# Performance work log

Measured on AMD Instinct MI355X. Metric: run time of the kernel, lower is better.

Reference implementation:

```python
import jax, jax.numpy as jnp
import numpy as np
from jax import lax

BLOCK = 20  # hardcoded block_size in BlockSparseSelfAttention
HEADS = 8
LAYERS = 4
EPS = 1e-5


def _ln(x, g, b):
    m = jnp.mean(x, axis=-1, keepdims=True)
    v = jnp.mean(jnp.square(x - m), axis=-1, keepdims=True)
    return (x - m) * lax.rsqrt(v + EPS) * g + b


def _conv1d(x_nct, w, b):
    # x: (B,C,T), w: (O,I,3) -> (B,O,T), padding=1 == SAME for k=3
    y = lax.conv_general_dilated(x_nct, w, (1,), 'SAME',
                                 dimension_numbers=('NCH', 'OIH', 'NCH'))
    return y + b[None, :, None]


def _block_attn(x, in_w, in_b, out_w, out_b):
    # torch nn.MultiheadAttention applied independently per length-BLOCK chunk
    B, T, D = x.shape
    nb, hd = T // BLOCK, D // HEADS
    xb = x.reshape(B, nb, BLOCK, D)
    qkv = jnp.einsum('bnsd,ed->bnse', xb, in_w) + in_b  # e = 3D
    q, k, v = jnp.split(qkv, 3, axis=-1)
    q = q.reshape(B, nb, BLOCK, HEADS, hd)
    k = k.reshape(B, nb, BLOCK, HEADS, hd)
    v = v.reshape(B, nb, BLOCK, HEADS, hd)
    scale = jnp.asarray(1.0 / np.sqrt(hd), x.dtype)
    s = jnp.einsum('bnqhd,bnkhd->bnhqk', q, k) * scale
    a = jax.nn.softmax(s, axis=-1)
    o = jnp.einsum('bnhqk,bnkhd->bnqhd', a, v).reshape(B, nb, BLOCK, D)
    o = jnp.einsum('bnsd,od->bnso', o, out_w) + out_b
    return o.reshape(B, T, D)


def setup_inputs() -> dict:
    key = jax.random.key(0)
    ks = iter(jax.random.split(key, 16))
    B, T, C, D, L = 32, 4000, 16, 256, LAYERS
    F = 4 * D
    s_c = 1.0 / np.sqrt(C * 3)
    s_d = 1.0 / np.sqrt(D)
    s_d3 = 1.0 / np.sqrt(D * 3)
    s_f = 1.0 / np.sqrt(F)
    f32 = jnp.float32
    return {
        'x': jax.random.normal(next(ks), (B, T, C), f32),
        'conv1_w': jax.random.normal(next(ks), (D, C, 3), f32) * s_c,
        'conv1_b': jnp.zeros((D,), f32),
        'conv2_w': jax.random.normal(next(ks), (D, D, 3), f32) * s_d3,
        'conv2_b': jnp.zeros((D,), f32),
        'ln_f_g': jnp.ones((D,), f32), 'ln_f_b': jnp.zeros((D,), f32),
        'trend_w': jax.random.normal(next(ks), (D, D), f32) * s_d,
        'trend_b': jnp.zeros((D,), f32),
        'season_w': jax.random.normal(next(ks), (D, D), f32) * s_d,
        'season_b': jnp.zeros((D,), f32),
        'attn_in_w': jax.random.normal(next(ks), (L, 3 * D, D), f32) * s_d,
        'attn_in_b': jnp.zeros((L, 3 * D), f32),
        'attn_out_w': jax.random.normal(next(ks), (L, D, D), f32) * s_d,
        'attn_out_b': jnp.zeros((L, D), f32),
        'ln1_g': jnp.ones((L, D), f32), 'ln1_b': jnp.zeros((L, D), f32),
        'ff1_w': jax.random.normal(next(ks), (L, F, D), f32) * s_d,
        'ff1_b': jnp.zeros((L, F), f32),
        'ff2_w': jax.random.normal(next(ks), (L, D, F), f32) * s_f,
        'ff2_b': jnp.zeros((L, D), f32),
        'ln2_g': jnp.ones((L, D), f32), 'ln2_b': jnp.zeros((L, D), f32),
        'fc_w': jax.random.normal(next(ks), (C, D), f32) * s_d,
        'fc_b': jnp.zeros((C,), f32),
    }


def reference(x, conv1_w, conv1_b, conv2_w, conv2_b, ln_f_g, ln_f_b,
              trend_w, trend_b, season_w, season_b,
              attn_in_w, attn_in_b, attn_out_w, attn_out_b,
              ln1_g, ln1_b, ff1_w, ff1_b, ff2_w, ff2_b, ln2_g, ln2_b,
              fc_w, fc_b):
    # FeatureExtractor
    h = x.transpose(0, 2, 1)                       # (B,C,T)
    h = jax.nn.relu(_conv1d(h, conv1_w, conv1_b))
    h = jax.nn.relu(_conv1d(h, conv2_w, conv2_b))
    h = h.transpose(0, 2, 1)                       # (B,T,D)
    h = _ln(h, ln_f_g, ln_f_b)
    # trend + seasonality residual
    h = h + (h @ trend_w.T + trend_b) + jnp.sin(h @ season_w.T + season_b)
    # encoder stack (dropout disabled / eval mode)
    for i in range(LAYERS):
        a = _block_attn(h, attn_in_w[i], attn_in_b[i], attn_out_w[i], attn_out_b[i])
        h = _ln(h + a, ln1_g[i], ln1_b[i])
        f = jax.nn.relu(h @ ff1_w[i].T + ff1_b[i]) @ ff2_w[i].T + ff2_b[i]
        h = _ln(h + f, ln2_g[i], ln2_b[i])
    return h[:, -1, :] @ fc_w.T + fc_b             # (B,C)
```

## Files before the change

### kernel.cpp

```cpp
#include <hip/hip_runtime.h>
#include <math.h>

typedef __attribute__((ext_vector_type(8))) short short8;
typedef __attribute__((ext_vector_type(4))) short short4v;
typedef __attribute__((ext_vector_type(4))) float f32x4;
typedef unsigned short ushort;
typedef unsigned int uint;
typedef unsigned long long u64;

#define MFMA16(a, b, c) __builtin_amdgcn_mfma_f32_16x16x32_bf16(a, b, c, 0, 0, 0)

__device__ __forceinline__ ushort f2bf(float f) {
  uint u = __float_as_uint(f);
  u = (u + 0x7FFFu + ((u >> 16) & 1u)) >> 16;
  return (ushort)u;
}
__device__ __forceinline__ int swz(int idx, int sh) {
  return idx ^ (((idx >> sh) & 7) << 3);
}
__device__ __forceinline__ float wsum(float v) {
#pragma unroll
  for (int off = 32; off > 0; off >>= 1) v += __shfl_xor(v, off, 64);
  return v;
}
__device__ __forceinline__ void gload16(short8& dst, const ushort* g) {
  u64 ga = (u64)g;
  asm volatile("global_load_dwordx4 %0, %1, off" : "=v"(dst) : "v"(ga));
}
__device__ __forceinline__ void vmw(int n) {
  if (n >= 7) asm volatile("s_waitcnt vmcnt(7)" ::: "memory");
  else if (n == 6) asm volatile("s_waitcnt vmcnt(6)" ::: "memory");
  else if (n == 5) asm volatile("s_waitcnt vmcnt(5)" ::: "memory");
  else if (n == 4) asm volatile("s_waitcnt vmcnt(4)" ::: "memory");
  else if (n == 3) asm volatile("s_waitcnt vmcnt(3)" ::: "memory");
  else if (n == 2) asm volatile("s_waitcnt vmcnt(2)" ::: "memory");
  else if (n == 1) asm volatile("s_waitcnt vmcnt(1)" ::: "memory");
  else asm volatile("s_waitcnt vmcnt(0)" ::: "memory");
}

#define S_CONV2 0
#define S_TREND 196608
#define S_SEASON 262144
#define S_QKV 327680
#define S_AOW 1114112
#define S_F1 1376256
#define S_F2 2424832
#define WTOT 3473408
#define O_C1G 3473408
#define O_C2O 3653632
#define O_G0 3981312
#define O_G1 4308992
#define O_PEND 4636672
#define O_QKV 4964352
#define O_FFB 5455872

template <int NCH>
__device__ __forceinline__ void dec2(int idx, int& row, int& k) {
  int pos = idx & 511, lane = pos >> 3, j = pos & 7;
  int kg = lane >> 4, col = lane & 15;
  int chunk = idx >> 9;
  int tile = chunk / (NCH * 4), r = chunk - tile * (NCH * 4);
  int kc = r >> 2, ks = r & 3;
  row = tile * 16 + col;
  k = kc * 128 + ks * 32 + kg * 8 + j;
}

__global__ void k_cvt(const float* __restrict__ c2w, const float* __restrict__ tw,
                      const float* __restrict__ sw, const float* __restrict__ aiw,
                      const float* __restrict__ aow, const float* __restrict__ f1w,
                      const float* __restrict__ f2w, ushort* __restrict__ ws) {
  for (int i = blockIdx.x * blockDim.x + threadIdx.x; i < WTOT;
       i += gridDim.x * blockDim.x) {
    float v; int row, k;
    if (i < S_TREND) {
      dec2<6>(i, row, k);
      int t = k >> 8, e = k & 255;
      v = c2w[row * 768 + e * 3 + t];
    } else if (i < S_SEASON) { dec2<2>(i - S_TREND, row, k); v = tw[row * 256 + k]; }
    else if (i < S_QKV) { dec2<2>(i - S_SEASON, row, k); v = sw[row * 256 + k]; }
    else if (i < S_AOW) {
      int r = i - S_QKV; int l = r / 196608; r -= l * 196608;
      dec2<2>(r, row, k); v = aiw[(size_t)l * 196608 + row * 256 + k];
    } else if (i < S_F1) {
      int r = i - S_AOW; int l = r >> 16; r &= 65535;
      dec2<2>(r, row, k); v = aow[l * 65536 + row * 256 + k];
    } else if (i < S_F2) {
      int r = i - S_F1; int l = r >> 18; r &= 262143;
      dec2<2>(r, row, k); v = f1w[l * 262144 + row * 256 + k];
    } else {
      int r = i - S_F2; int l = r >> 18; r &= 262143;
      dec2<8>(r, row, k); v = f2w[l * 262144 + row * 1024 + k];
    }
    ws[i] = f2bf(v);
  }
}

template <int NCH, int MY, int ASH>
__device__ __forceinline__ void ring_gemm(const ushort* __restrict__ A, int lda,
                                          const ushort* __restrict__ ws0,
                                          int lane, f32x4 (&acc)[MY][2]) {
  constexpr int C = MY * NCH * 4;
  constexpr int R = (C < 8) ? C : 8;
  const int col = lane & 15, kg = lane >> 4;
  const int r1c = (16 + col > 19) ? 19 : (16 + col);
  short8 rg[R];
#pragma unroll
  for (int r = 0; r < R; ++r) gload16(rg[r], ws0 + r * 512);
  short8 af0[4], af1[4];
#pragma unroll
  for (int c = 0; c < C; ++c) {
    const int i = c / (NCH * 4), r = c - i * (NCH * 4);
    const int kc = r >> 2, ks = r & 3;
    if (ks == 0) {
#pragma unroll
      for (int s = 0; s < 4; ++s) {
        const int k0 = kc * 128 + s * 32 + kg * 8;
        af0[s] = *(const short8*)(A + swz(col * lda + k0, ASH));
        af1[s] = *(const short8*)(A + swz(r1c * lda + k0, ASH));
      }
    }
    int allow = C - 1 - c; if (allow > R - 1) allow = R - 1;
    vmw(allow);
    __builtin_amdgcn_sched_barrier(0);
    acc[i][0] = MFMA16(af0[ks], rg[c % R], acc[i][0]);
    acc[i][1] = MFMA16(af1[ks], rg[c % R], acc[i][1]);
    if (c + R < C) gload16(rg[c % R], ws0 + (c + R) * 512);
  }
}

__device__ __forceinline__ void stage_b16(const ushort* __restrict__ g, ushort* hb,
                                          int n, int sh, int tid) {
  for (int i = tid * 8; i < n; i += 2048) {
    short8 v = *(const short8*)(g + i);
    *(short8*)(hb + swz(i, sh)) = v;
  }
}
__device__ __forceinline__ void stage_f32(const float* __restrict__ g, ushort* hb, int tid) {
  for (int i = tid * 8; i < 5120; i += 2048) {
    float4 a = *(const float4*)(g + i);
    float4 b = *(const float4*)(g + i + 4);
    short8 t;
    t[0] = f2bf(a.x); t[1] = f2bf(a.y); t[2] = f2bf(a.z); t[3] = f2bf(a.w);
    t[4] = f2bf(b.x); t[5] = f2bf(b.y); t[6] = f2bf(b.z); t[7] = f2bf(b.w);
    *(short8*)(hb + swz(i, 8)) = t;
  }
}
__device__ __forceinline__ void stage_ln(const float* __restrict__ g1,
                                         const float* __restrict__ pend,
                                         const float* __restrict__ gam,
                                         const float* __restrict__ bet,
                                         ushort* hb, float* __restrict__ gout,
                                         float* f32lds, int tid) {
  const int lane = tid & 63, w = tid >> 6, d0 = lane * 4;
  for (int r = w; r < 20; r += 4) {
    float4 a = *(const float4*)(g1 + r * 256 + d0);
    if (pend) {
      float4 p = *(const float4*)(pend + r * 256 + d0);
      a.x += p.x; a.y += p.y; a.z += p.z; a.w += p.w;
    }
    float m = wsum(a.x + a.y + a.z + a.w) * (1.f / 256.f);
    float c0 = a.x - m, c1 = a.y - m, c2 = a.z - m, c3 = a.w - m;
    float var = wsum(c0 * c0 + c1 * c1 + c2 * c2 + c3 * c3) * (1.f / 256.f);
    float inv = rsqrtf(var + 1e-5f);
    float o0 = c0 * inv * gam[d0] + bet[d0];
    float o1 = c1 * inv * gam[d0 + 1] + bet[d0 + 1];
    float o2 = c2 * inv * gam[d0 + 2] + bet[d0 + 2];
    float o3 = c3 * inv * gam[d0 + 3] + bet[d0 + 3];
    short4v t; t[0] = f2bf(o0); t[1] = f2bf(o1); t[2] = f2bf(o2); t[3] = f2bf(o3);
    *(short4v*)(hb + swz(r * 256 + d0, 8)) = t;
    if (gout) { float4 o = {o0, o1, o2, o3}; *(float4*)(gout + r * 256 + d0) = o; }
    if (f32lds) { float4 o = {o0, o1, o2, o3}; *(float4*)(f32lds + r * 256 + d0) = o; }
  }
}

__global__ __launch_bounds__(256) void k_conv1(const float* __restrict__ x,
                                               const float* __restrict__ c1w,
                                               const float* __restrict__ c1b,
                                               ushort* __restrict__ c1g) {
  __shared__ float xs[24][16];
  const int tid = threadIdx.x, b = blockIdx.x;
  for (int i = tid; i < 24 * 16; i += 256) {
    int r = i >> 4, c = i & 15;
    xs[r][c] = (r < 23) ? x[((size_t)b * 4000 + 3977 + r) * 16 + c] : 0.f;
  }
  __syncthreads();
  const int d = tid;
  const float* wr = c1w + d * 48;
  float acc[21];
  const float bv = c1b[d];
#pragma unroll
  for (int r = 0; r < 21; ++r) acc[r] = bv;
  for (int c = 0; c < 16; ++c) {
    float xv[23];
#pragma unroll
    for (int i = 0; i < 23; ++i) xv[i] = xs[i + 1][c];
    float w0 = wr[c * 3], w1 = wr[c * 3 + 1], w2 = wr[c * 3 + 2];
#pragma unroll
    for (int r = 0; r < 21; ++r)
      acc[r] += xv[r] * w0 + xv[r + 1] * w1 + xv[r + 2] * w2;
  }
  ushort* o = c1g + b * 5632;
#pragma unroll
  for (int r = 0; r < 21; ++r) o[r * 256 + d] = f2bf(fmaxf(acc[r], 0.f));
  o[21 * 256 + d] = 0;
}

__global__ __launch_bounds__(256, 2) void k_conv2(const ushort* __restrict__ c1g,
                                                  const ushort* __restrict__ wst,
                                                  const float* __restrict__ c2b,
                                                  float* __restrict__ c2o) {
  __shared__ __align__(16) ushort hb[5632];
  const int tid = threadIdx.x, lane = tid & 63, wv = tid >> 6;
  const int b = blockIdx.x >> 2, slice = blockIdx.x & 3;
  const int col = lane & 15, kg = lane >> 4;
  stage_b16(c1g + b * 5632, hb, 5632, 8, tid);
  const int tile = slice * 4 + wv, og = tile * 16 + col;
  float bv = c2b[og];
  __syncthreads();
  asm volatile("s_waitcnt vmcnt(0)" ::: "memory");
  f32x4 acc[1][2];
  acc[0][0] = {bv, bv, bv, bv}; acc[0][1] = {bv, bv, bv, bv};
  ring_gemm<6, 1, 8>(hb, 256, wst + tile * 12288 + lane * 8, lane, acc);
  float* ob = c2o + b * 5120;
#pragma unroll
  for (int mt = 0; mt < 2; ++mt)
#pragma unroll
    for (int j = 0; j < 4; ++j) {
      int row = mt * 16 + kg * 4 + j;
      if (row < 20) ob[row * 256 + og] = fmaxf(acc[0][mt][j], 0.f);
    }
}

__global__ __launch_bounds__(256, 2) void k_tresea(
    const float* __restrict__ c2o, const ushort* __restrict__ wtr,
    const ushort* __restrict__ wse, const float* __restrict__ lnfg,
    const float* __restrict__ lnfb, const float* __restrict__ tb,
    const float* __restrict__ sb, float* __restrict__ g0) {
  __shared__ __align__(16) ushort hb[5120];
  __shared__ float hf[5120];
  const int tid = threadIdx.x, lane = tid & 63, wv = tid >> 6;
  const int b = blockIdx.x >> 2, slice = blockIdx.x & 3;
  const int col = lane & 15, kg = lane >> 4;
  stage_ln(c2o + b * 5120, nullptr, lnfg, lnfb, hb, nullptr, hf, tid);
  const int tile = slice * 4 + wv, og = tile * 16 + col;
  float bt = tb[og], bs = sb[og];
  __syncthreads();
  asm volatile("s_waitcnt vmcnt(0)" ::: "memory");
  f32x4 at[1][2], as_[1][2];
  at[0][0] = {bt, bt, bt, bt}; at[0][1] = {bt, bt, bt, bt};
  as_[0][0] = {bs, bs, bs, bs}; as_[0][1] = {bs, bs, bs, bs};
  ring_gemm<2, 1, 8>(hb, 256, wtr + tile * 4096 + lane * 8, lane, at);
  ring_gemm<2, 1, 8>(hb, 256, wse + tile * 4096 + lane * 8, lane, as_);
  float* ob = g0 + b * 5120;
#pragma unroll
  for (int mt = 0; mt < 2; ++mt)
#pragma unroll
    for (int j = 0; j < 4; ++j) {
      int row = mt * 16 + kg * 4 + j;
      if (row < 20)
        ob[row * 256 + og] = hf[row * 256 + og] + at[0][mt][j] + sinf(as_[0][mt][j]);
    }
}

__global__ __launch_bounds__(256, 2) void k_qkv(
    const float* __restrict__ gin, const float* __restrict__ pend,
    const float* __restrict__ lng, const float* __restrict__ lnb, int fuse_ln,
    float* __restrict__ gout, const ushort* __restrict__ wst,
    const float* __restrict__ bias, ushort* __restrict__ qkvo) {
  __shared__ __align__(16) ushort hb[5120];
  const int tid = threadIdx.x, lane = tid & 63, wv = tid >> 6;
  const int b = blockIdx.x / 12, slice = blockIdx.x % 12;
  const int col = lane & 15, kg = lane >> 4;
  if (fuse_ln)
    stage_ln(gin + b * 5120, pend + b * 5120, lng, lnb, hb,
             (slice == 0) ? (gout + b * 5120) : nullptr, nullptr, tid);
  else
    stage_f32(gin + b * 5120, hb, tid);
  const int tile = slice * 4 + wv, og = tile * 16 + col;
  float bv = bias[og];
  __syncthreads();
  asm volatile("s_waitcnt vmcnt(0)" ::: "memory");
  f32x4 acc[1][2];
  acc[0][0] = {bv, bv, bv, bv}; acc[0][1] = {bv, bv, bv, bv};
  ring_gemm<2, 1, 8>(hb, 256, wst + tile * 4096 + lane * 8, lane, acc);
  ushort* ob = qkvo + b * 15360;
#pragma unroll
  for (int mt = 0; mt < 2; ++mt)
#pragma unroll
    for (int j = 0; j < 4; ++j) {
      int row = mt * 16 + kg * 4 + j;
      if (row < 20) ob[row * 768 + og] = f2bf(acc[0][mt][j]);
    }
}

__global__ __launch_bounds__(256, 2) void k_attnaow(
    const ushort* __restrict__ qkvo, const ushort* __restrict__ wst,
    const float* __restrict__ bias, float* __restrict__ pend) {
  __shared__ __align__(16) ushort qb[15360];
  __shared__ __align__(16) ushort vT[8192];
  __shared__ __align__(16) ushort Pb[5120];
  __shared__ __align__(16) ushort aob[5120];
  __shared__ float sc[3200];
  const int tid = threadIdx.x, lane = tid & 63, wv = tid >> 6;
  const int b = blockIdx.x >> 2, slice = blockIdx.x & 3;
  const int col = lane & 15, kg = lane >> 4;
  const int r1c = (16 + col > 19) ? 19 : (16 + col);
  stage_b16(qkvo + b * 15360, qb, 15360, 8, tid);
  __syncthreads();
  for (int i = tid; i < 8192; i += 256) {
    int hh = i >> 10, rem = i & 1023, dh = rem >> 5, tk = rem & 31;
    ushort v = (tk < 20) ? qb[swz(tk * 768 + 512 + hh * 32 + dh, 8)] : (ushort)0;
    vT[swz(i, 5)] = v;
  }
  __syncthreads();
  for (int hh = wv; hh < 8; hh += 4) {
    short8 aq[2], bk[2];
    aq[0] = *(const short8*)(qb + swz(col * 768 + hh * 32 + kg * 8, 8));
    aq[1] = *(const short8*)(qb + swz(r1c * 768 + hh * 32 + kg * 8, 8));
    bk[0] = *(const short8*)(qb + swz(col * 768 + 256 + hh * 32 + kg * 8, 8));
    bk[1] = *(const short8*)(qb + swz(r1c * 768 + 256 + hh * 32 + kg * 8, 8));
    f32x4 d[2][2];
#pragma unroll
    for (int mt = 0; mt < 2; ++mt)
#pragma unroll
      for (int nt = 0; nt < 2; ++nt) {
        d[mt][nt] = {0.f, 0.f, 0.f, 0.f};
        d[mt][nt] = MFMA16(aq[mt], bk[nt], d[mt][nt]);
      }
#pragma unroll
    for (int mt = 0; mt < 2; ++mt)
#pragma unroll
      for (int nt = 0; nt < 2; ++nt)
#pragma unroll
        for (int j = 0; j < 4; ++j) {
          int row = mt * 16 + kg * 4 + j, kj = nt * 16 + col;
          if (row < 20 && kj < 20)
            sc[hh * 400 + row * 20 + kj] = d[mt][nt][j] * 0.17677669529663687f;
        }
  }
  __syncthreads();
  if (tid < 160) {
    const int hh = tid / 20, q = tid - hh * 20;
    const float* row = sc + hh * 400 + q * 20;
    float m = row[0];
#pragma unroll
    for (int j = 1; j < 20; ++j) m = fmaxf(m, row[j]);
    float e[20], s = 0.f;
#pragma unroll
    for (int j = 0; j < 20; ++j) { e[j] = __expf(row[j] - m); s += e[j]; }
    float inv = 1.f / s;
#pragma unroll
    for (int j = 0; j < 20; ++j) Pb[swz(hh * 640 + q * 32 + j, 5)] = f2bf(e[j] * inv);
#pragma unroll
    for (int j = 20; j < 32; ++j) Pb[swz(hh * 640 + q * 32 + j, 5)] = 0;
  }
  __syncthreads();
  for (int hh = wv; hh < 8; hh += 4) {
    short8 ap[2], bvv[2];
    ap[0] = *(const short8*)(Pb + swz(hh * 640 + col * 32 + kg * 8, 5));
    ap[1] = *(const short8*)(Pb + swz(hh * 640 + r1c * 32 + kg * 8, 5));
    bvv[0] = *(const short8*)(vT + swz(hh * 1024 + col * 32 + kg * 8, 5));
    bvv[1] = *(const short8*)(vT + swz(hh * 1024 + (16 + col) * 32 + kg * 8, 5));
    f32x4 d[2][2];
#pragma unroll
    for (int mt = 0; mt < 2; ++mt)
#pragma unroll
      for (int nt = 0; nt < 2; ++nt) {
        d[mt][nt] = {0.f, 0.f, 0.f, 0.f};
        d[mt][nt] = MFMA16(ap[mt], bvv[nt], d[mt][nt]);
      }
#pragma unroll
    for (int mt = 0; mt < 2; ++mt)
#pragma unroll
      for (int nt = 0; nt < 2; ++nt)
#pragma unroll
        for (int j = 0; j < 4; ++j) {
          int row = mt * 16 + kg * 4 + j, dc = nt * 16 + col;
          if (row < 20) aob[swz(row * 256 + hh * 32 + dc, 8)] = f2bf(d[mt][nt][j]);
        }
  }
  __syncthreads();
  const int tile = slice * 4 + wv, og = tile * 16 + col;
  float bv = bias[og];
  asm volatile("s_waitcnt vmcnt(0)" ::: "memory");
  f32x4 acc[1][2];
  acc[0][0] = {bv, bv, bv, bv}; acc[0][1] = {bv, bv, bv, bv};
  ring_gemm<2, 1, 8>(aob, 256, wst + tile * 4096 + lane * 8, lane, acc);
  float* ob = pend + b * 5120;
#pragma unroll
  for (int mt = 0; mt < 2; ++mt)
#pragma unroll
    for (int j = 0; j < 4; ++j) {
      int row = mt * 16 + kg * 4 + j;
      if (row < 20) ob[row * 256 + og] = acc[0][mt][j];
    }
}

__global__ __launch_bounds__(256, 2) void k_ff1(
    const float* __restrict__ g0, const float* __restrict__ pend,
    const float* __restrict__ lng, const float* __restrict__ lnb,
    float* __restrict__ g1, const ushort* __restrict__ wst,
    const float* __restrict__ bias, ushort* __restrict__ ffbo) {
  __shared__ __align__(16) ushort hb[5120];
  const int tid = threadIdx.x, lane = tid & 63, wv = tid >> 6;
  const int b = blockIdx.x >> 3, slice = blockIdx.x & 7;
  const int col = lane & 15, kg = lane >> 4;
  stage_ln(g0 + b * 5120, pend + b * 5120, lng, lnb, hb,
           (slice == 0) ? (g1 + b * 5120) : nullptr, nullptr, tid);
  const int t0 = slice * 8 + wv * 2;
  float bv0 = bias[t0 * 16 + col], bv1 = bias[(t0 + 1) * 16 + col];
  __syncthreads();
  asm volatile("s_waitcnt vmcnt(0)" ::: "memory");
  f32x4 acc[2][2];
  acc[0][0] = {bv0, bv0, bv0, bv0}; acc[0][1] = {bv0, bv0, bv0, bv0};
  acc[1][0] = {bv1, bv1, bv1, bv1}; acc[1][1] = {bv1, bv1, bv1, bv1};
  ring_gemm<2, 2, 8>(hb, 256, wst + t0 * 4096 + lane * 8, lane, acc);
  ushort* ob = ffbo + b * 20480;
#pragma unroll
  for (int i = 0; i < 2; ++i) {
    const int og = (t0 + i) * 16 + col;
#pragma unroll
    for (int mt = 0; mt < 2; ++mt)
#pragma unroll
      for (int j = 0; j < 4; ++j) {
        int row = mt * 16 + kg * 4 + j;
        if (row < 20) ob[row * 1024 + og] = f2bf(fmaxf(acc[i][mt][j], 0.f));
      }
  }
}

__global__ __launch_bounds__(256, 2) void k_ff2(const ushort* __restrict__ ffbo,
                                                const ushort* __restrict__ wst,
                                                const float* __restrict__ bias,
                                                float* __restrict__ pend) {
  __shared__ __align__(16) ushort hb[20480];
  const int tid = threadIdx.x, lane = tid & 63, wv = tid >> 6;
  const int b = blockIdx.x >> 2, slice = blockIdx.x & 3;
  const int col = lane & 15, kg = lane >> 4;
  stage_b16(ffbo + b * 20480, hb, 20480, 10, tid);
  const int tile = slice * 4 + wv, og = tile * 16 + col;
  float bv = bias[og];
  __syncthreads();
  asm volatile("s_waitcnt vmcnt(0)" ::: "memory");
  f32x4 acc[1][2];
  acc[0][0] = {bv, bv, bv, bv}; acc[0][1] = {bv, bv, bv, bv};
  ring_gemm<8, 1, 10>(hb, 1024, wst + tile * 16384 + lane * 8, lane, acc);
  float* ob = pend + b * 5120;
#pragma unroll
  for (int mt = 0; mt < 2; ++mt)
#pragma unroll
    for (int j = 0; j < 4; ++j) {
      int row = mt * 16 + kg * 4 + j;
      if (row < 20) ob[row * 256 + og] = acc[0][mt][j];
    }
}

__global__ __launch_bounds__(256) void k_fc(
    const float* __restrict__ g1, const float* __restrict__ pend,
    const float* __restrict__ lng, const float* __restrict__ lnb,
    const float* __restrict__ fcw, const float* __restrict__ fcb,
    float* __restrict__ out) {
  __shared__ float hn[256];
  const int tid = threadIdx.x, b = blockIdx.x;
  if (tid < 64) {
    const int d0 = tid * 4;
    float4 a = *(const float4*)(g1 + b * 5120 + 19 * 256 + d0);
    float4 p = *(const float4*)(pend + b * 5120 + 19 * 256 + d0);
    a.x += p.x; a.y += p.y; a.z += p.z; a.w += p.w;
    float m = wsum(a.x + a.y + a.z + a.w) * (1.f / 256.f);
    float c0 = a.x - m, c1 = a.y - m, c2 = a.z - m, c3 = a.w - m;
    float var = wsum(c0 * c0 + c1 * c1 + c2 * c2 + c3 * c3) * (1.f / 256.f);
    float inv = rsqrtf(var + 1e-5f);
    hn[d0] = c0 * inv * lng[d0] + lnb[d0];
    hn[d0 + 1] = c1 * inv * lng[d0 + 1] + lnb[d0 + 1];
    hn[d0 + 2] = c2 * inv * lng[d0 + 2] + lnb[d0 + 2];
    hn[d0 + 3] = c3 * inv * lng[d0 + 3] + lnb[d0 + 3];
  }
  __syncthreads();
  const int g = tid >> 4, t = tid & 15;
  float s = 0.f;
#pragma unroll
  for (int j = 0; j < 16; ++j) {
    int k = t * 16 + j;
    s += hn[k] * fcw[g * 256 + k];
  }
#pragma unroll
  for (int off = 1; off < 16; off <<= 1) s += __shfl_xor(s, off, 64);
  if (t == 0) out[b * 16 + g] = s + fcb[g];
}

extern "C" void kernel_launch(void* const* d_in, const int* in_sizes, int n_in,
                              void* d_out, int out_size, void* d_ws, size_t ws_size,
                              hipStream_t stream) {
  const float* x    = (const float*)d_in[0];
  const float* c1w  = (const float*)d_in[1];
  const float* c1b  = (const float*)d_in[2];
  const float* c2w  = (const float*)d_in[3];
  const float* c2b  = (const float*)d_in[4];
  const float* lnfg = (const float*)d_in[5];
  const float* lnfb = (const float*)d_in[6];
  const float* tw   = (const float*)d_in[7];
  const float* tb   = (const float*)d_in[8];
  const float* sw   = (const float*)d_in[9];
  const float* sb   = (const float*)d_in[10];
  const float* aiw  = (const float*)d_in[11];
  const float* aib  = (const float*)d_in[12];
  const float* aow  = (const float*)d_in[13];
  const float* aobb = (const float*)d_in[14];
  const float* l1g  = (const float*)d_in[15];
  const float* l1b  = (const float*)d_in[16];
  const float* f1w  = (const float*)d_in[17];
  const float* f1b  = (const float*)d_in[18];
  const float* f2w  = (const float*)d_in[19];
  const float* f2b  = (const float*)d_in[20];
  const float* l2g  = (const float*)d_in[21];
  const float* l2b  = (const float*)d_in[22];
  const float* fcw  = (const float*)d_in[23];
  const float* fcb  = (const float*)d_in[24];
  float* out = (float*)d_out;
  ushort* ws = (ushort*)d_ws;

  ushort* c1g  = ws + O_C1G;
  float* c2o   = (float*)(ws + O_C2O);
  float* g0    = (float*)(ws + O_G0);
  float* g1    = (float*)(ws + O_G1);
  float* pend  = (float*)(ws + O_PEND);
  ushort* qkvo = ws + O_QKV;
  ushort* ffbo = ws + O_FFB;

  k_cvt<<<4096, 256, 0, stream>>>(c2w, tw, sw, aiw, aow, f1w, f2w, ws);
  k_conv1<<<32, 256, 0, stream>>>(x, c1w, c1b, c1g);
  k_conv2<<<128, 256, 0, stream>>>(c1g, ws + S_CONV2, c2b, c2o);
  k_tresea<<<128, 256, 0, stream>>>(c2o, ws + S_TREND, ws + S_SEASON, lnfg,
                                    lnfb, tb, sb, g0);
  for (int l = 0; l < 4; ++l) {
    k_qkv<<<384, 256, 0, stream>>>(
        l == 0 ? g0 : g1, pend, l ? l2g + (l - 1) * 256 : nullptr,
        l ? l2b + (l - 1) * 256 : nullptr, l ? 1 : 0, g0,
        ws + S_QKV + l * 196608, aib + l * 768, qkvo);
    k_attnaow<<<128, 256, 0, stream>>>(qkvo, ws + S_AOW + l * 65536,
                                       aobb + l * 256, pend);
    k_ff1<<<256, 256, 0, stream>>>(g0, pend, l1g + l * 256, l1b + l * 256, g1,
                                   ws + S_F1 + l * 262144, f1b + l * 1024,
                                   ffbo);
    k_ff2<<<128, 256, 0, stream>>>(ffbo, ws + S_F2 + l * 262144, f2b + l * 256,
                                   pend);
  }
  k_fc<<<32, 256, 0, stream>>>(g1, pend, l2g + 3 * 256, l2b + 3 * 256, fcw,
                               fcb, out);
}
```

Baseline: 154.8 us.

## Fuse conv1 into conv2 and attention+out-proj+LN1 into FF1 kernel

Merges the conv1 and conv2 kernels so conv1 output goes straight to shared memory instead of a global bf16 buffer. Also fuses attention, the output projection, residual+LayerNorm1 and FF1 into one kernel launched with 256 blocks. Each of the 8 slices per batch recomputes the full attention and full output projection redundantly, trading extra compute and lower occupancy (launch bounds 1) for fewer launches and no global round-trip through pend. Conv1 is likewise recomputed by 4 slices per batch.

```diff
diff --git a/kernel.cpp b/kernel.cpp
--- a/kernel.cpp
+++ b/kernel.cpp
@@ -46,7 +46,6 @@
 #define S_F1 1376256
 #define S_F2 2424832
 #define WTOT 3473408
-#define O_C1G 3473408
 #define O_C2O 3653632
 #define O_G0 3981312
 #define O_G1 4308992
@@ -173,61 +172,55 @@
   }
 }
 
-__global__ __launch_bounds__(256) void k_conv1(const float* __restrict__ x,
-                                               const float* __restrict__ c1w,
-                                               const float* __restrict__ c1b,
-                                               ushort* __restrict__ c1g) {
+__global__ __launch_bounds__(256, 2) void k_conv12(
+    const float* __restrict__ x, const float* __restrict__ c1w,
+    const float* __restrict__ c1b, const ushort* __restrict__ wst,
+    const float* __restrict__ c2b, float* __restrict__ c2o) {
   __shared__ float xs[24][16];
-  const int tid = threadIdx.x, b = blockIdx.x;
+  __shared__ __align__(16) ushort c1u[5632];
+  const int tid = threadIdx.x, lane = tid & 63, wv = tid >> 6;
+  const int b = blockIdx.x >> 2, slice = blockIdx.x & 3;
+  const int col = lane & 15, kg = lane >> 4;
   for (int i = tid; i < 24 * 16; i += 256) {
     int r = i >> 4, c = i & 15;
     xs[r][c] = (r < 23) ? x[((size_t)b * 4000 + 3977 + r) * 16 + c] : 0.f;
   }
   __syncthreads();
-  const int d = tid;
-  const float* wr = c1w + d * 48;
-  float acc[21];
-  const float bv = c1b[d];
-#pragma unroll
-  for (int r = 0; r < 21; ++r) acc[r] = bv;
-  for (int c = 0; c < 16; ++c) {
-    float xv[23];
-#pragma unroll
-    for (int i = 0; i < 23; ++i) xv[i] = xs[i + 1][c];
-    float w0 = wr[c * 3], w1 = wr[c * 3 + 1], w2 = wr[c * 3 + 2];
+  {
+    const int d = tid;
+    const float* wr = c1w + d * 48;
+    float acc[21];
+    const float bv = c1b[d];
+#pragma unroll
+    for (int r = 0; r < 21; ++r) acc[r] = bv;
+    for (int c = 0; c < 16; ++c) {
+      float xv[23];
+#pragma unroll
+      for (int i = 0; i < 23; ++i) xv[i] = xs[i + 1][c];
+      float w0 = wr[c * 3], w1 = wr[c * 3 + 1], w2 = wr[c * 3 + 2];
+#pragma unroll
+      for (int r = 0; r < 21; ++r)
+        acc[r] += xv[r] * w0 + xv[r + 1] * w1 + xv[r + 2] * w2;
+    }
 #pragma unroll
     for (int r = 0; r < 21; ++r)
-      acc[r] += xv[r] * w0 + xv[r + 1] * w1 + xv[r + 2] * w2;
-  }
-  ushort* o = c1g + b * 5632;
-#pragma unroll
-  for (int r = 0; r < 21; ++r) o[r * 256 + d] = f2bf(fmaxf(acc[r], 0.f));
-  o[21 * 256 + d] = 0;
-}
-
-__global__ __launch_bounds__(256, 2) void k_conv2(const ushort* __restrict__ c1g,
-                                                  const ushort* __restrict__ wst,
-                                                  const float* __restrict__ c2b,
-                                                  float* __restrict__ c2o) {
-  __shared__ __align__(16) ushort hb[5632];
-  const int tid = threadIdx.x, lane = tid & 63, wv = tid >> 6;
-  const int b = blockIdx.x >> 2, slice = blockIdx.x & 3;
-  const int col = lane & 15, kg = lane >> 4;
-  stage_b16(c1g + b * 5632, hb, 5632, 8, tid);
+      c1u[swz(r * 256 + d, 8)] = f2bf(fmaxf(acc[r], 0.f));
+    c1u[swz(21 * 256 + d, 8)] = 0;
+  }
   const int tile = slice * 4 + wv, og = tile * 16 + col;
-  float bv = c2b[og];
+  float bv2 = c2b[og];
   __syncthreads();
   asm volatile("s_waitcnt vmcnt(0)" ::: "memory");
-  f32x4 acc[1][2];
-  acc[0][0] = {bv, bv, bv, bv}; acc[0][1] = {bv, bv, bv, bv};
-  ring_gemm<6, 1, 8>(hb, 256, wst + tile * 12288 + lane * 8, lane, acc);
+  f32x4 acc2[1][2];
+  acc2[0][0] = {bv2, bv2, bv2, bv2}; acc2[0][1] = {bv2, bv2, bv2, bv2};
+  ring_gemm<6, 1, 8>(c1u, 256, wst + tile * 12288 + lane * 8, lane, acc2);
   float* ob = c2o + b * 5120;
 #pragma unroll
   for (int mt = 0; mt < 2; ++mt)
 #pragma unroll
     for (int j = 0; j < 4; ++j) {
       int row = mt * 16 + kg * 4 + j;
-      if (row < 20) ob[row * 256 + og] = fmaxf(acc[0][mt][j], 0.f);
+      if (row < 20) ob[row * 256 + og] = fmaxf(acc2[0][mt][j], 0.f);
     }
 }
 
@@ -293,18 +286,24 @@
     }
 }
 
-__global__ __launch_bounds__(256, 2) void k_attnaow(
-    const ushort* __restrict__ qkvo, const ushort* __restrict__ wst,
-    const float* __restrict__ bias, float* __restrict__ pend) {
+__global__ __launch_bounds__(256, 1) void k_aff1(
+    const ushort* __restrict__ qkvo, const ushort* __restrict__ waow,
+    const float* __restrict__ aobb, const float* __restrict__ g0,
+    const float* __restrict__ l1g, const float* __restrict__ l1b,
+    float* __restrict__ g1, const ushort* __restrict__ wf1,
+    const float* __restrict__ f1b, ushort* __restrict__ ffbo) {
   __shared__ __align__(16) ushort qb[15360];
   __shared__ __align__(16) ushort vT[8192];
   __shared__ __align__(16) ushort Pb[5120];
   __shared__ __align__(16) ushort aob[5120];
   __shared__ float sc[3200];
+  __shared__ __align__(16) ushort hb[5120];
+  float* proj = (float*)qb;
   const int tid = threadIdx.x, lane = tid & 63, wv = tid >> 6;
-  const int b = blockIdx.x >> 2, slice = blockIdx.x & 3;
+  const int b = blockIdx.x >> 3, slice = blockIdx.x & 7;
   const int col = lane & 15, kg = lane >> 4;
   const int r1c = (16 + col > 19) ? 19 : (16 + col);
+
   stage_b16(qkvo + b * 15360, qb, 15360, 8, tid);
   __syncthreads();
   for (int i = tid; i < 8192; i += 256) {
@@ -380,52 +379,79 @@
         }
   }
   __syncthreads();
-  const int tile = slice * 4 + wv, og = tile * 16 + col;
-  float bv = bias[og];
-  asm volatile("s_waitcnt vmcnt(0)" ::: "memory");
-  f32x4 acc[1][2];
-  acc[0][0] = {bv, bv, bv, bv}; acc[0][1] = {bv, bv, bv, bv};
-  ring_gemm<2, 1, 8>(aob, 256, wst + tile * 4096 + lane * 8, lane, acc);
-  float* ob = pend + b * 5120;
-#pragma unroll
-  for (int mt = 0; mt < 2; ++mt)
-#pragma unroll
-    for (int j = 0; j < 4; ++j) {
-      int row = mt * 16 + kg * 4 + j;
-      if (row < 20) ob[row * 256 + og] = acc[0][mt][j];
-    }
-}
-
-__global__ __launch_bounds__(256, 2) void k_ff1(
-    const float* __restrict__ g0, const float* __restrict__ pend,
-    const float* __restrict__ lng, const float* __restrict__ lnb,
-    float* __restrict__ g1, const ushort* __restrict__ wst,
-    const float* __restrict__ bias, ushort* __restrict__ ffbo) {
-  __shared__ __align__(16) ushort hb[5120];
-  const int tid = threadIdx.x, lane = tid & 63, wv = tid >> 6;
-  const int b = blockIdx.x >> 3, slice = blockIdx.x & 7;
-  const int col = lane & 15, kg = lane >> 4;
-  stage_ln(g0 + b * 5120, pend + b * 5120, lng, lnb, hb,
-           (slice == 0) ? (g1 + b * 5120) : nullptr, nullptr, tid);
-  const int t0 = slice * 8 + wv * 2;
-  float bv0 = bias[t0 * 16 + col], bv1 = bias[(t0 + 1) * 16 + col];
-  __syncthreads();
-  asm volatile("s_waitcnt vmcnt(0)" ::: "memory");
-  f32x4 acc[2][2];
-  acc[0][0] = {bv0, bv0, bv0, bv0}; acc[0][1] = {bv0, bv0, bv0, bv0};
-  acc[1][0] = {bv1, bv1, bv1, bv1}; acc[1][1] = {bv1, bv1, bv1, bv1};
-  ring_gemm<2, 2, 8>(hb, 256, wst + t0 * 4096 + lane * 8, lane, acc);
-  ushort* ob = ffbo + b * 20480;
-#pragma unroll
-  for (int i = 0; i < 2; ++i) {
-    const int og = (t0 + i) * 16 + col;
-#pragma unroll
-    for (int mt = 0; mt < 2; ++mt)
-#pragma unroll
-      for (int j = 0; j < 4; ++j) {
-        int row = mt * 16 + kg * 4 + j;
-        if (row < 20) ob[row * 1024 + og] = f2bf(fmaxf(acc[i][mt][j], 0.f));
+
+  {
+    float bo[4];
+#pragma unroll
+    for (int i = 0; i < 4; ++i) bo[i] = aobb[(wv * 4 + i) * 16 + col];
+    asm volatile("s_waitcnt vmcnt(0)" ::: "memory");
+    f32x4 acc[4][2];
+#pragma unroll
+    for (int i = 0; i < 4; ++i) {
+      acc[i][0] = {bo[i], bo[i], bo[i], bo[i]};
+      acc[i][1] = {bo[i], bo[i], bo[i], bo[i]};
+    }
+    ring_gemm<2, 4, 8>(aob, 256, waow + (wv * 4) * 4096 + lane * 8, lane, acc);
+#pragma unroll
+    for (int i = 0; i < 4; ++i) {
+      const int og = (wv * 4 + i) * 16 + col;
+#pragma unroll
+      for (int mt = 0; mt < 2; ++mt)
+#pragma unroll
+        for (int j = 0; j < 4; ++j) {
+          int row = mt * 16 + kg * 4 + j;
+          if (row < 20) proj[row * 256 + og] = acc[i][mt][j];
+        }
+    }
+  }
+  __syncthreads();
+
+  {
+    const int d0 = lane * 4;
+    for (int r = wv; r < 20; r += 4) {
+      float4 a = *(const float4*)(g0 + b * 5120 + r * 256 + d0);
+      a.x += proj[r * 256 + d0];
+      a.y += proj[r * 256 + d0 + 1];
+      a.z += proj[r * 256 + d0 + 2];
+      a.w += proj[r * 256 + d0 + 3];
+      float m = wsum(a.x + a.y + a.z + a.w) * (1.f / 256.f);
+      float c0 = a.x - m, c1 = a.y - m, c2 = a.z - m, c3 = a.w - m;
+      float var = wsum(c0 * c0 + c1 * c1 + c2 * c2 + c3 * c3) * (1.f / 256.f);
+      float inv = rsqrtf(var + 1e-5f);
+      float o0 = c0 * inv * l1g[d0] + l1b[d0];
+      float o1 = c1 * inv * l1g[d0 + 1] + l1b[d0 + 1];
+      float o2 = c2 * inv * l1g[d0 + 2] + l1b[d0 + 2];
+      float o3 = c3 * inv * l1g[d0 + 3] + l1b[d0 + 3];
+      short4v t; t[0] = f2bf(o0); t[1] = f2bf(o1); t[2] = f2bf(o2); t[3] = f2bf(o3);
+      *(short4v*)(hb + swz(r * 256 + d0, 8)) = t;
+      if (slice == 0) {
+        float4 o = {o0, o1, o2, o3};
+        *(float4*)(g1 + b * 5120 + r * 256 + d0) = o;
       }
+    }
+  }
+  __syncthreads();
+
+  {
+    const int t0 = slice * 8 + wv * 2;
+    float bf0 = f1b[t0 * 16 + col], bf1 = f1b[(t0 + 1) * 16 + col];
+    asm volatile("s_waitcnt vmcnt(0)" ::: "memory");
+    f32x4 acc[2][2];
+    acc[0][0] = {bf0, bf0, bf0, bf0}; acc[0][1] = {bf0, bf0, bf0, bf0};
+    acc[1][0] = {bf1, bf1, bf1, bf1}; acc[1][1] = {bf1, bf1, bf1, bf1};
+    ring_gemm<2, 2, 8>(hb, 256, wf1 + t0 * 4096 + lane * 8, lane, acc);
+    ushort* ob = ffbo + b * 20480;
+#pragma unroll
+    for (int i = 0; i < 2; ++i) {
+      const int og = (t0 + i) * 16 + col;
+#pragma unroll
+      for (int mt = 0; mt < 2; ++mt)
+#pragma unroll
+        for (int j = 0; j < 4; ++j) {
+          int row = mt * 16 + kg * 4 + j;
+          if (row < 20) ob[row * 1024 + og] = f2bf(fmaxf(acc[i][mt][j], 0.f));
+        }
+    }
   }
 }
 
@@ -520,7 +546,6 @@
   float* out = (float*)d_out;
   ushort* ws = (ushort*)d_ws;
 
-  ushort* c1g  = ws + O_C1G;
   float* c2o   = (float*)(ws + O_C2O);
   float* g0    = (float*)(ws + O_G0);
   float* g1    = (float*)(ws + O_G1);
@@ -529,8 +554,7 @@
   ushort* ffbo = ws + O_FFB;
 
   k_cvt<<<4096, 256, 0, stream>>>(c2w, tw, sw, aiw, aow, f1w, f2w, ws);
-  k_conv1<<<32, 256, 0, stream>>>(x, c1w, c1b, c1g);
-  k_conv2<<<128, 256, 0, stream>>>(c1g, ws + S_CONV2, c2b, c2o);
+  k_conv12<<<128, 256, 0, stream>>>(x, c1w, c1b, ws + S_CONV2, c2b, c2o);
   k_tresea<<<128, 256, 0, stream>>>(c2o, ws + S_TREND, ws + S_SEASON, lnfg,
                                     lnfb, tb, sb, g0);
   for (int l = 0; l < 4; ++l) {
@@ -538,11 +562,10 @@
         l == 0 ? g0 : g1, pend, l ? l2g + (l - 1) * 256 : nullptr,
         l ? l2b + (l - 1) * 256 : nullptr, l ? 1 : 0, g0,
         ws + S_QKV + l * 196608, aib + l * 768, qkvo);
-    k_attnaow<<<128, 256, 0, stream>>>(qkvo, ws + S_AOW + l * 65536,
-                                       aobb + l * 256, pend);
-    k_ff1<<<256, 256, 0, stream>>>(g0, pend, l1g + l * 256, l1b + l * 256, g1,
-                                   ws + S_F1 + l * 262144, f1b + l * 1024,
-                                   ffbo);
+    k_aff1<<<256, 256, 0, stream>>>(qkvo, ws + S_AOW + l * 65536,
+                                    aobb + l * 256, g0, l1g + l * 256,
+                                    l1b + l * 256, g1, ws + S_F1 + l * 262144,
+                                    f1b + l * 1024, ffbo);
     k_ff2<<<128, 256, 0, stream>>>(ffbo, ws + S_F2 + l * 262144, f2b + l * 256,
                                    pend);
   }
```

New measurement: 149.3 us. 3.5% less time.
